# Kernel tuning notes

Measured on AMD Instinct MI355X. Metric: run time of the kernel, lower is better.

The kernel has to match this reference:

```python
import jax, jax.numpy as jnp
import numpy as np

N = 65536      # nodes
M = 65536      # memory nodes (== N, so no padding branch)
D = 256        # dim_model
H = 8          # heads
DK = D // H    # 32
DFF = 1024
E1 = 1048576   # intra edges
E2 = 524288    # inter edges
MAX_ETYPE = 1000
EPS = 1e-5
SCALE = 1.0 / float(np.sqrt(DK))


def layer_norm(x, g, b):
    mu = jnp.mean(x, axis=-1, keepdims=True)
    var = jnp.mean((x - mu) ** 2, axis=-1, keepdims=True)
    return (x - mu) * jax.lax.rsqrt(var + EPS) * g + b


def graph_attention(q, k, v, src, dst, n_dst, e_rel=None):
    # q: [Nq,H,DK]; k,v: [Nk,H,DK]; src/dst: [E]
    e = jnp.einsum('ehd,ehd->eh', k[src], q[dst])  # masked_mm
    if e_rel is not None:
        e = e + e_rel                               # node_mul_edge bias
    e = e * SCALE
    # segment softmax over incoming edges per destination (sparse_softmax)
    m = jax.ops.segment_max(e, dst, num_segments=n_dst)
    ex = jnp.exp(e - m[dst])
    denom = jax.ops.segment_sum(ex, dst, num_segments=n_dst)
    a = ex / denom[dst]                             # [E,H]
    # vec_spmm: aggregate a * v[src] into dst
    return jax.ops.segment_sum(a[:, :, None] * v[src], dst, num_segments=n_dst)


def setup_inputs() -> dict:
    key = jax.random.key(0)
    ks = jax.random.split(key, 24)
    w = lambda k, shp, fan: jax.random.normal(k, shp, jnp.float32) * (1.0 / np.sqrt(fan))
    inp = {
        'h': jax.random.normal(ks[0], (N, D), jnp.float32),
        'mem': jax.random.normal(ks[1], (M, D), jnp.float32),
        'src_intra': jax.random.randint(ks[2], (E1,), 0, N, jnp.int32),
        'dst_intra': jax.random.randint(ks[3], (E1,), 0, N, jnp.int32),
        'etype': jax.random.randint(ks[4], (E1,), 0, MAX_ETYPE, jnp.int32),
        'src_inter': jax.random.randint(ks[5], (E2,), 0, M, jnp.int32),
        'dst_inter': jax.random.randint(ks[6], (E2,), 0, N, jnp.int32),
        # intra-attention projections (branch 0)
        'Wq0': w(ks[7], (D, D), D), 'Wk0': w(ks[8], (D, D), D),
        'Wv0': w(ks[9], (D, D), D), 'Wo0': w(ks[10], (D, D), D),
        # inter-attention projections (branch 1)
        'Wq1': w(ks[11], (D, D), D), 'Wk1': w(ks[12], (D, D), D),
        'Wv1': w(ks[13], (D, D), D), 'Wo1': w(ks[14], (D, D), D),
        'ak_embed': jax.random.normal(ks[15], (MAX_ETYPE, DK), jnp.float32) * 0.02,
        # layer norms: norm_in[0], norm_in[1], norm_inter
        'ln0_g': jnp.ones((D,), jnp.float32), 'ln0_b': jnp.zeros((D,), jnp.float32),
        'ln1_g': jnp.ones((D,), jnp.float32), 'ln1_b': jnp.zeros((D,), jnp.float32),
        'ln2_g': jnp.ones((D,), jnp.float32), 'ln2_b': jnp.zeros((D,), jnp.float32),
        # FFN
        'Wf1': w(ks[16], (D, DFF), D), 'bf1': jnp.zeros((DFF,), jnp.float32),
        'Wf2': w(ks[17], (DFF, D), DFF), 'bf2': jnp.zeros((D,), jnp.float32),
    }
    return inp


def reference(h, mem, Wq0, Wk0, Wv0, Wo0, Wq1, Wk1, Wv1, Wo1, ak_embed,
              ln0_g, ln0_b, ln1_g, ln1_b, ln2_g, ln2_b,
              Wf1, bf1, Wf2, bf2,
              src_intra, dst_intra, etype, src_inter, dst_inter):
    # ---- intra (self) graph attention ----
    q = (h @ Wq0).reshape(-1, H, DK)
    k = (h @ Wk0).reshape(-1, H, DK)
    v = (h @ Wv0).reshape(-1, H, DK)
    ak = ak_embed[etype]                                   # [E1, DK]
    e_rel = jnp.einsum('ed,ehd->eh', ak, q[dst_intra])     # rel-pos bias
    a = graph_attention(q, k, v, src_intra, dst_intra, N, e_rel)
    o = a.reshape(-1, D) @ Wo0
    h = layer_norm(h + o, ln0_g, ln0_b)
    # ---- inter (memory) graph attention ----  (M == N: no padding)
    q = (h @ Wq1).reshape(-1, H, DK)
    k = (mem @ Wk1).reshape(-1, H, DK)
    v = (mem @ Wv1).reshape(-1, H, DK)
    a = graph_attention(q, k, v, src_inter, dst_inter, N)
    o = a.reshape(-1, D) @ Wo1
    h = layer_norm(h + o, ln1_g, ln1_b)
    # ---- FFN + norm_inter ----
    ffn = jax.nn.relu(h @ Wf1 + bf1) @ Wf2 + bf2
    h = layer_norm(h + ffn, ln2_g, ln2_b)
    return h
```

## Files before the change

### kernel.cpp

```cpp
#include <hip/hip_runtime.h>

#define N_NODES 65536
#define D_MODEL 256
#define DFF     1024
#define E1_N    1048576
#define E2_N    524288
#define ATT_SCALE 0.17677669529663687f
#define LN_EPS  1e-5f

#define NBUCK   128
#define BSHIFT  9
#define DPB     512

typedef __attribute__((ext_vector_type(8))) __bf16 bf16x8;
typedef __attribute__((ext_vector_type(4))) float  floatx4;
typedef __attribute__((ext_vector_type(4))) unsigned short ushortx4;
typedef __attribute__((ext_vector_type(8))) unsigned short ushortx8;

__device__ __forceinline__ float bf2f(unsigned short u) {
  return __uint_as_float(((unsigned)u) << 16);
}
__device__ __forceinline__ unsigned short f2bf(float f) {
  unsigned u = __float_as_uint(f);
  return (unsigned short)((u + 0x7FFFu + ((u >> 16) & 1u)) >> 16);
}
__device__ __forceinline__ int dot4i8(unsigned a, unsigned b, int c) {
#if __has_builtin(__builtin_amdgcn_sdot4)
  return __builtin_amdgcn_sdot4((int)a, (int)b, c, false);
#else
  c += (int)(signed char)(a & 0xFF) * (int)(signed char)(b & 0xFF);
  c += (int)(signed char)((a >> 8) & 0xFF) * (int)(signed char)((b >> 8) & 0xFF);
  c += (int)(signed char)((a >> 16) & 0xFF) * (int)(signed char)((b >> 16) & 0xFF);
  c += (int)(signed char)(a >> 24) * (int)(signed char)(b >> 24);
  return c;
#endif
}
__device__ __forceinline__ unsigned pack4i8(float a, float b, float c, float d, float inv) {
  int r0 = __float2int_rn(a * inv) & 0xFF;
  int r1 = __float2int_rn(b * inv) & 0xFF;
  int r2 = __float2int_rn(c * inv) & 0xFF;
  int r3 = __float2int_rn(d * inv) & 0xFF;
  return (unsigned)(r0 | (r1 << 8) | (r2 << 16) | (r3 << 24));
}

__device__ __forceinline__ void gld_lds16(const void* g, void* l) {
  __builtin_amdgcn_global_load_lds(
      (const __attribute__((address_space(1))) unsigned int*)g,
      (__attribute__((address_space(3))) unsigned int*)l, 16, 0, 0);
}

struct TW8 {
  const float* w[8];
  unsigned short* o[8];
};
__global__ __launch_bounds__(256) void transpose8(TW8 t) {
  __shared__ float tile[32][33];
  const int z = blockIdx.z;
  const float* W = t.w[z];
  unsigned short* Wt = t.o[z];
  const int tx = threadIdx.x & 31;
  const int ty = threadIdx.x >> 5;
  const int r0 = blockIdx.y * 32;
  const int c0 = blockIdx.x * 32;
#pragma unroll
  for (int p = 0; p < 4; ++p) {
    const int r = ty + p * 8;
    tile[r][tx] = W[(size_t)(r0 + r) * 256 + c0 + tx];
  }
  __syncthreads();
#pragma unroll
  for (int p = 0; p < 4; ++p) {
    const int r = ty + p * 8;
    Wt[(size_t)(c0 + r) * 256 + r0 + tx] = f2bf(tile[tx][r]);
  }
}

__global__ __launch_bounds__(256) void transpose_w(const float* __restrict__ W,
                                                   unsigned short* __restrict__ Wt,
                                                   int K, int Nc) {
  __shared__ float tile[32][33];
  const int tx = threadIdx.x & 31;
  const int ty = threadIdx.x >> 5;
  const int r0 = blockIdx.y * 32;
  const int c0 = blockIdx.x * 32;
#pragma unroll
  for (int p = 0; p < 4; ++p) {
    const int r = ty + p * 8;
    tile[r][tx] = W[(size_t)(r0 + r) * Nc + c0 + tx];
  }
  __syncthreads();
#pragma unroll
  for (int p = 0; p < 4; ++p) {
    const int r = ty + p * 8;
    Wt[(size_t)(c0 + r) * K + r0 + tx] = f2bf(tile[tx][r]);
  }
}

__global__ __launch_bounds__(256) void f2bf2_kernel(const float* __restrict__ in0,
                                                    unsigned short* __restrict__ out0,
                                                    const float* __restrict__ in1,
                                                    unsigned short* __restrict__ out1,
                                                    int half) {
  int i = blockIdx.x * 256 + threadIdx.x;
  const float* in = (i < half) ? in0 : in1;
  unsigned short* out = (i < half) ? out0 : out1;
  int k = (i < half) ? i : i - half;
  float4 v = ((const float4*)in)[k];
  ushortx4 o;
  o.x = f2bf(v.x); o.y = f2bf(v.y); o.z = f2bf(v.z); o.w = f2bf(v.w);
  ((ushortx4*)out)[k] = o;
}

__global__ __launch_bounds__(256) void zero_kernel(int* __restrict__ p, int n) {
  int i = blockIdx.x * 256 + threadIdx.x;
  if (i < n) p[i] = 0;
}


__global__ __launch_bounds__(256) void bucket_hist_kernel(const int* __restrict__ d0,
                                                          int* __restrict__ bh0,
                                                          const int* __restrict__ d1,
                                                          int* __restrict__ bh1) {
  __shared__ int h0[NBUCK], h1[NBUCK];
  const int tid = threadIdx.x;
  if (tid < NBUCK) { h0[tid] = 0; h1[tid] = 0; }
  __syncthreads();
  const int base = blockIdx.x * 2048;
#pragma unroll
  for (int i = 0; i < 8; ++i) {
    const int e = base + i * 256 + tid;
    atomicAdd(&h0[d0[e] >> BSHIFT], 1);
    if (e < E2_N) atomicAdd(&h1[d1[e] >> BSHIFT], 1);
  }
  __syncthreads();
  if (tid < NBUCK) {
    if (h0[tid]) atomicAdd(&bh0[tid], h0[tid]);
  } else if (tid < 2 * NBUCK) {
    const int t = tid - NBUCK;
    if (h1[t]) atomicAdd(&bh1[t], h1[t]);
  }
}

__global__ __launch_bounds__(256) void bucket_scan_kernel(const int* __restrict__ bh0,
                                                          int* __restrict__ bs0,
                                                          int* __restrict__ bc0,
                                                          int* __restrict__ rs0,
                                                          const int* __restrict__ bh1,
                                                          int* __restrict__ bs1,
                                                          int* __restrict__ bc1,
                                                          int* __restrict__ rs1) {
  __shared__ int l[2][NBUCK];
  const int tid = threadIdx.x;
  const int g = tid >> 7;
  const int t = tid & 127;
  const int* bh = g ? bh1 : bh0;
  int* bs = g ? bs1 : bs0;
  int* bc = g ? bc1 : bc0;
  const int orig = bh[t];
  int v = orig;
  l[g][t] = v;
  __syncthreads();
  for (int off = 1; off < NBUCK; off <<= 1) {
    const int add = (t >= off) ? l[g][t - off] : 0;
    __syncthreads();
    v += add;
    l[g][t] = v;
    __syncthreads();
  }
  bs[t + 1] = v;
  bc[t] = v - orig;
  if (t == 0) bs[0] = 0;
  if (tid == 0) rs0[N_NODES] = E1_N;
  if (tid == 1) rs1[N_NODES] = E2_N;
}

template <bool INTRA>
__global__ __launch_bounds__(256) void bin_kernel(const int* __restrict__ src,
                                                  const int* __restrict__ dst,
                                                  const int* __restrict__ et,
                                                  int* __restrict__ bcur,
                                                  void* __restrict__ outv) {
  __shared__ int cnt[NBUCK], gbase[NBUCK], lcur[NBUCK];
  const int tid = threadIdx.x;
  const int base = blockIdx.x * 2048;
  if (tid < NBUCK) { cnt[tid] = 0; lcur[tid] = 0; }
  int d[8], bk[8];
#pragma unroll
  for (int i = 0; i < 8; ++i) d[i] = dst[base + i * 256 + tid];
  __syncthreads();
#pragma unroll
  for (int i = 0; i < 8; ++i) {
    bk[i] = d[i] >> BSHIFT;
    atomicAdd(&cnt[bk[i]], 1);
  }
  __syncthreads();
  if (tid < NBUCK) gbase[tid] = atomicAdd(&bcur[tid], cnt[tid]);
  __syncthreads();
  if (INTRA) {
    int2* out = (int2*)outv;
#pragma unroll
    for (int i = 0; i < 8; ++i) {
      const int e = base + i * 256 + tid;
      const int loc = atomicAdd(&lcur[bk[i]], 1);
      out[gbase[bk[i]] + loc] = make_int2(src[e], (d[i] & (DPB - 1)) | (et[e] << 16));
    }
  } else {
    int* out = (int*)outv;
#pragma unroll
    for (int i = 0; i < 8; ++i) {
      const int e = base + i * 256 + tid;
      const int loc = atomicAdd(&lcur[bk[i]], 1);
      out[gbase[bk[i]] + loc] = src[e] | ((d[i] & (DPB - 1)) << 16);
    }
  }
}

__global__ __launch_bounds__(256) void csr_build_kernel(const int2* __restrict__ binned0,
                                                        const int* __restrict__ bs0,
                                                        int* __restrict__ rs0,
                                                        int2* __restrict__ out0,
                                                        const int* __restrict__ binned1,
                                                        const int* __restrict__ bs1,
                                                        int* __restrict__ rs1,
                                                        int* __restrict__ out1) {
  __shared__ int cnt[DPB];
  __shared__ int cur[DPB];
  __shared__ int wsum[4];
  const int tid = threadIdx.x;
  const int g = blockIdx.x >> 7;
  const int b = blockIdx.x & 127;
  const int bb = g ? bs1[b] : bs0[b];
  const int be = g ? bs1[b + 1] : bs0[b + 1];
  cnt[tid] = 0;
  cnt[tid + 256] = 0;
  __syncthreads();
  if (g == 0) {
    for (int j = bb + tid; j < be; j += 256) {
      atomicAdd(&cnt[binned0[j].y & (DPB - 1)], 1);
    }
  } else {
    for (int j = bb + tid; j < be; j += 256) {
      atomicAdd(&cnt[binned1[j] >> 16], 1);
    }
  }
  __syncthreads();
  const int lane = tid & 63;
  const int wv = tid >> 6;
  const int c0 = cnt[2 * tid];
  const int c1 = cnt[2 * tid + 1];
  const int s = c0 + c1;
  int incl = s;
#pragma unroll
  for (int m = 1; m < 64; m <<= 1) {
    const int u = __shfl_up(incl, m);
    if (lane >= m) incl += u;
  }
  if (lane == 63) wsum[wv] = incl;
  __syncthreads();
  int wb = 0;
  for (int w = 0; w < wv; ++w) wb += wsum[w];
  const int e0 = bb + wb + (incl - s);
  int* rs = g ? rs1 : rs0;
  rs[(b << BSHIFT) + 2 * tid] = e0;
  rs[(b << BSHIFT) + 2 * tid + 1] = e0 + c0;
  cur[2 * tid] = e0;
  cur[2 * tid + 1] = e0 + c0;
  __syncthreads();
  if (g == 0) {
    for (int j = bb + tid; j < be; j += 256) {
      const int2 w = binned0[j];
      const int p = atomicAdd(&cur[w.y & (DPB - 1)], 1);
      out0[p] = make_int2(w.x, w.y >> 16);
    }
  } else {
    for (int j = bb + tid; j < be; j += 256) {
      const int w = binned1[j];
      const int p = atomicAdd(&cur[w >> 16], 1);
      out1[p] = w & 0xFFFF;
    }
  }
}

template <bool BIAS, bool RELU, bool OUT_KVQ>
__global__ __launch_bounds__(256) void gemm_bf16(const unsigned short* __restrict__ A,
                                                 const unsigned short* __restrict__ Bt,
                                                 const float* __restrict__ bias,
                                                 void* __restrict__ C,
                                                 float* __restrict__ sbuf,
                                                 int K, int Ntot) {
  __shared__ __align__(16) unsigned short sA[128 * 32];
  __shared__ __align__(16) unsigned short sB[128 * 32];
  const int tid  = threadIdx.x;
  const int wave = tid >> 6;
  const int lane = tid & 63;
  const int m0 = blockIdx.y * 128;
  const int n0 = blockIdx.x * 128;

  floatx4 acc[4][4] = {};

  const int l4r = lane >> 2;
  const int l4c = (lane & 3) * 8;
  const int fr = lane & 15;
  const int fk = (lane >> 4) * 8;
  const int wy = (wave >> 1) * 64;
  const int wx = (wave & 1) * 64;

  for (int k0 = 0; k0 < K; k0 += 32) {
#pragma unroll
    for (int c = 0; c < 2; ++c) {
      const int row = wave * 32 + c * 16;
      gld_lds16(A  + ((size_t)(m0 + row + l4r) * K + k0 + l4c), &sA[row * 32]);
      gld_lds16(Bt + ((size_t)(n0 + row + l4r) * K + k0 + l4c), &sB[row * 32]);
    }
    __syncthreads();
    bf16x8 af[4], bfv[4];
#pragma unroll
    for (int i = 0; i < 4; ++i) af[i]  = *(const bf16x8*)&sA[(wy + i * 16 + fr) * 32 + fk];
#pragma unroll
    for (int j = 0; j < 4; ++j) bfv[j] = *(const bf16x8*)&sB[(wx + j * 16 + fr) * 32 + fk];
#pragma unroll
    for (int i = 0; i < 4; ++i)
#pragma unroll
      for (int j = 0; j < 4; ++j)
        acc[i][j] = __builtin_amdgcn_mfma_f32_16x16x32_bf16(af[i], bfv[j], acc[i][j], 0, 0, 0);
    __syncthreads();
  }

  const int coln = lane & 15;
  const int rowq = (lane >> 4) * 4;

  if (OUT_KVQ) {
    unsigned char* Cb = (unsigned char*)C;
#pragma unroll
    for (int i = 0; i < 4; ++i) {
#pragma unroll
      for (int jp = 0; jp < 2; ++jp) {
        const int head = ((n0 + wx) >> 5) + jp;
        const int pidx = (head < 8) ? head * 2 : (head - 8) * 2 + 1;
#pragma unroll
        for (int r = 0; r < 4; ++r) {
          float am = fmaxf(fabsf(acc[i][2 * jp][r]), fabsf(acc[i][2 * jp + 1][r]));
          am = fmaxf(am, __shfl_xor(am, 1));
          am = fmaxf(am, __shfl_xor(am, 2));
          am = fmaxf(am, __shfl_xor(am, 4));
          am = fmaxf(am, __shfl_xor(am, 8));
          const int m = m0 + wy + i * 16 + rowq + r;
          const float inv = am > 0.f ? 127.f / am : 0.f;
#pragma unroll
          for (int jj = 0; jj < 2; ++jj) {
            const int j = 2 * jp + jj;
            const int n = n0 + wx + j * 16 + coln;
            const int qv = __float2int_rn(acc[i][j][r] * inv);
            Cb[(size_t)m * 512 + n] = (unsigned char)(signed char)qv;
          }
          if (coln == 0) {
            sbuf[(size_t)m * 16 + pidx] = am * (1.f / 127.f);
          }
        }
      }
    }
  } else {
    unsigned short* Cs = (unsigned short*)C;
#pragma unroll
    for (int j = 0; j < 4; ++j) {
      const int n = n0 + wx + j * 16 + coln;
      float bval = 0.f;
      if (BIAS) bval = bias[n];
#pragma unroll
      for (int i = 0; i < 4; ++i) {
        const int mbase = m0 + wy + i * 16 + rowq;
#pragma unroll
        for (int r = 0; r < 4; ++r) {
          float v = acc[i][j][r] + bval;
          if (RELU) v = fmaxf(v, 0.f);
          Cs[(size_t)(mbase + r) * Ntot + n] = f2bf(v);
        }
      }
    }
  }
}

template <bool HAS_REL>
__global__ __launch_bounds__(256) void attn_kernel(const unsigned short* qb,
                                                   const unsigned char* __restrict__ kvb,
                                                   const float* __restrict__ sbuf,
                                                   const int* __restrict__ row_start,
                                                   const int2* __restrict__ s_se,
                                                   const int* __restrict__ s_src,
                                                   const float* __restrict__ ak_embed,
                                                   unsigned short* outp) {
  const int lane = threadIdx.x & 63;
  const int wave = threadIdx.x >> 6;
  const int dst  = blockIdx.x * 4 + wave;
  const int eg   = lane >> 4;
  const int l    = lane & 15;
  const int doff = l * 16;

  const unsigned short* qrow = qb + (size_t)dst * 256 + doff;
  ushortx8 qu0 = *(const ushortx8*)qrow;
  ushortx8 qu1 = *(const ushortx8*)(qrow + 8);
  float q[16];
#pragma unroll
  for (int d = 0; d < 8; ++d) {
    q[d]     = bf2f(qu0[d]) * ATT_SCALE;
    q[d + 8] = bf2f(qu1[d]) * ATT_SCALE;
  }
  float qam = 0.f;
#pragma unroll
  for (int d = 0; d < 16; ++d) qam = fmaxf(qam, fabsf(q[d]));
  qam = fmaxf(qam, __shfl_xor(qam, 1));
  const float qs   = qam * (1.f / 127.f);
  const float qinv = qam > 0.f ? 127.f / qam : 0.f;
  unsigned qi[4];
#pragma unroll
  for (int c = 0; c < 4; ++c)
    qi[c] = pack4i8(q[4 * c], q[4 * c + 1], q[4 * c + 2], q[4 * c + 3], qinv);

  float a[16];
#pragma unroll
  for (int d = 0; d < 16; ++d) a[d] = 0.f;
  float lsum = 0.f;

  const int beg = row_start[dst], end = row_start[dst + 1];
  for (int j = beg; j < end; j += 4) {
    const int e = j + eg;
    const bool valid = e < end;
    const int ecl = valid ? e : (end - 1);
    int src, et = 0;
    if (HAS_REL) {
      int2 se = s_se[ecl];
      src = se.x; et = se.y;
    } else {
      src = s_src[ecl];
    }
    const unsigned char* kvrow = kvb + (size_t)src * 512;
    float2 sc = *(const float2*)(sbuf + (size_t)src * 16 + (l >> 1) * 2);
    uint4 ku = *(const uint4*)(kvrow + doff);
    uint4 vu = *(const uint4*)(kvrow + 256 + doff);
    int idot = 0;
    idot = dot4i8(ku.x, qi[0], idot);
    idot = dot4i8(ku.y, qi[1], idot);
    idot = dot4i8(ku.z, qi[2], idot);
    idot = dot4i8(ku.w, qi[3], idot);
    float part = (float)idot * (sc.x * qs);
    if (HAS_REL) {
      const float* ak = ak_embed + (size_t)et * 32 + (l & 1) * 16;
      float4 a0 = *(const float4*)ak;
      float4 a1 = *(const float4*)(ak + 4);
      float4 a2 = *(const float4*)(ak + 8);
      float4 a3 = *(const float4*)(ak + 12);
      part += a0.x * q[0]  + a0.y * q[1]  + a0.z * q[2]  + a0.w * q[3]
            + a1.x * q[4]  + a1.y * q[5]  + a1.z * q[6]  + a1.w * q[7]
            + a2.x * q[8]  + a2.y * q[9]  + a2.z * q[10] + a2.w * q[11]
            + a3.x * q[12] + a3.y * q[13] + a3.z * q[14] + a3.w * q[15];
    }
    part += __shfl_xor(part, 1);
    const float pw = valid ? __expf(part) : 0.f;
    lsum += pw;
    const float pwv = pw * sc.y;
    {
      unsigned u = vu.x;
      a[0] += pwv * (float)(signed char)(u & 0xFF);
      a[1] += pwv * (float)(signed char)((u >> 8) & 0xFF);
      a[2] += pwv * (float)(signed char)((u >> 16) & 0xFF);
      a[3] += pwv * (float)(signed char)(u >> 24);
      u = vu.y;
      a[4] += pwv * (float)(signed char)(u & 0xFF);
      a[5] += pwv * (float)(signed char)((u >> 8) & 0xFF);
      a[6] += pwv * (float)(signed char)((u >> 16) & 0xFF);
      a[7] += pwv * (float)(signed char)(u >> 24);
      u = vu.z;
      a[8]  += pwv * (float)(signed char)(u & 0xFF);
      a[9]  += pwv * (float)(signed char)((u >> 8) & 0xFF);
      a[10] += pwv * (float)(signed char)((u >> 16) & 0xFF);
      a[11] += pwv * (float)(signed char)(u >> 24);
      u = vu.w;
      a[12] += pwv * (float)(signed char)(u & 0xFF);
      a[13] += pwv * (float)(signed char)((u >> 8) & 0xFF);
      a[14] += pwv * (float)(signed char)((u >> 16) & 0xFF);
      a[15] += pwv * (float)(signed char)(u >> 24);
    }
  }
  lsum += __shfl_xor(lsum, 16);
  lsum += __shfl_xor(lsum, 32);
#pragma unroll
  for (int d = 0; d < 16; ++d) {
    a[d] += __shfl_xor(a[d], 16);
    a[d] += __shfl_xor(a[d], 32);
  }
  const float inv = lsum > 0.f ? 1.f / lsum : 0.f;
  if (eg == 0) {
    ushortx8 o0, o1;
#pragma unroll
    for (int d = 0; d < 8; ++d) {
      o0[d] = f2bf(a[d] * inv);
      o1[d] = f2bf(a[d + 8] * inv);
    }
    unsigned short* orow = outp + (size_t)dst * 256 + doff;
    *(ushortx8*)orow = o0;
    *(ushortx8*)(orow + 8) = o1;
  }
}

template <bool WRITE_BF>
__global__ __launch_bounds__(256) void ln_kernel(const float* __restrict__ xin,
                                                 const unsigned short* __restrict__ oin,
                                                 const float* __restrict__ g,
                                                 const float* __restrict__ b,
                                                 float* __restrict__ xout,
                                                 unsigned short* __restrict__ bfout) {
  const int lane = threadIdx.x & 63;
  const int wave = threadIdx.x >> 6;
  const size_t row  = (size_t)blockIdx.x * 4 + wave;
  const size_t base = row * 256 + lane * 4;
  float4 xv = *(const float4*)(xin + base);
  ushortx4 ou = *(const ushortx4*)(oin + base);
  const float x0 = xv.x + bf2f(ou.x), x1 = xv.y + bf2f(ou.y),
              x2 = xv.z + bf2f(ou.z), x3 = xv.w + bf2f(ou.w);
  float sum = x0 + x1 + x2 + x3;
  float ss  = x0 * x0 + x1 * x1 + x2 * x2 + x3 * x3;
#pragma unroll
  for (int m = 1; m <= 32; m <<= 1) {
    sum += __shfl_xor(sum, m);
    ss  += __shfl_xor(ss, m);
  }
  const float mu  = sum * (1.f / 256.f);
  const float var = ss * (1.f / 256.f) - mu * mu;
  const float rs  = rsqrtf(var + LN_EPS);
  float4 gv = *(const float4*)(g + lane * 4);
  float4 bv = *(const float4*)(b + lane * 4);
  const float y0 = (x0 - mu) * rs * gv.x + bv.x;
  const float y1 = (x1 - mu) * rs * gv.y + bv.y;
  const float y2 = (x2 - mu) * rs * gv.z + bv.z;
  const float y3 = (x3 - mu) * rs * gv.w + bv.w;
  *(float4*)(xout + base) = make_float4(y0, y1, y2, y3);
  if (WRITE_BF) {
    ushortx4 yo;
    yo.x = f2bf(y0); yo.y = f2bf(y1); yo.z = f2bf(y2); yo.w = f2bf(y3);
    *(ushortx4*)(bfout + base) = yo;
  }
}

extern "C" void kernel_launch(void* const* d_in, const int* in_sizes, int n_in,
                              void* d_out, int out_size, void* d_ws, size_t ws_size,
                              hipStream_t stream) {
  const float* h_in      = (const float*)d_in[0];
  const float* mem_in    = (const float*)d_in[1];
  const int*   src_intra = (const int*)d_in[2];
  const int*   dst_intra = (const int*)d_in[3];
  const int*   etype     = (const int*)d_in[4];
  const int*   src_inter = (const int*)d_in[5];
  const int*   dst_inter = (const int*)d_in[6];
  const float* Wq0 = (const float*)d_in[7];
  const float* Wk0 = (const float*)d_in[8];
  const float* Wv0 = (const float*)d_in[9];
  const float* Wo0 = (const float*)d_in[10];
  const float* Wq1 = (const float*)d_in[11];
  const float* Wk1 = (const float*)d_in[12];
  const float* Wv1 = (const float*)d_in[13];
  const float* Wo1 = (const float*)d_in[14];
  const float* akE = (const float*)d_in[15];
  const float* ln0_g = (const float*)d_in[16];
  const float* ln0_b = (const float*)d_in[17];
  const float* ln1_g = (const float*)d_in[18];
  const float* ln1_b = (const float*)d_in[19];
  const float* ln2_g = (const float*)d_in[20];
  const float* ln2_b = (const float*)d_in[21];
  const float* Wf1 = (const float*)d_in[22];
  const float* bf1 = (const float*)d_in[23];
  const float* Wf2 = (const float*)d_in[24];
  const float* bf2 = (const float*)d_in[25];

  char* p = (char*)d_ws;
  auto alloc = [&](size_t bytes) {
    char* r = p;
    p += (bytes + 255) & ~(size_t)255;
    return r;
  };

  unsigned short* wqkv0t = (unsigned short*)alloc((size_t)768 * 256 * 2);
  unsigned short* wo0t   = (unsigned short*)alloc((size_t)256 * 256 * 2);
  unsigned short* wq1t   = (unsigned short*)alloc((size_t)256 * 256 * 2);
  unsigned short* wkv1t  = (unsigned short*)alloc((size_t)512 * 256 * 2);
  unsigned short* wo1t   = (unsigned short*)alloc((size_t)256 * 256 * 2);
  unsigned short* wf1t   = (unsigned short*)alloc((size_t)1024 * 256 * 2);
  unsigned short* wf2t   = (unsigned short*)alloc((size_t)256 * 1024 * 2);

  int* rs0   = (int*)alloc((size_t)(N_NODES + 1) * 4);
  int* rs1   = (int*)alloc((size_t)(N_NODES + 1) * 4);
  int2* sse0 = (int2*)alloc((size_t)E1_N * 8);
  int* ssrc1 = (int*)alloc((size_t)E2_N * 4);
  int* bh01 = (int*)alloc((size_t)2 * NBUCK * 4);
  int* bh0 = bh01;
  int* bh1 = bh01 + NBUCK;
  int* bs0 = (int*)alloc((size_t)(NBUCK + 1) * 4);
  int* bs1 = (int*)alloc((size_t)(NBUCK + 1) * 4);
  int* bc0 = (int*)alloc((size_t)NBUCK * 4);
  int* bc1 = (int*)alloc((size_t)NBUCK * 4);

  char* regionA = alloc((size_t)128 * 1024 * 1024);
  int2* binned0 = (int2*)regionA;
  int*  binned1 = (int*)(regionA + (size_t)E1_N * 8);
  unsigned short* qbuf    = (unsigned short*)regionA;
  unsigned char*  kv0q    = (unsigned char*)(regionA + (size_t)33554432);
  unsigned char*  kv1q    = (unsigned char*)(regionA + (size_t)67108864);
  unsigned short* scratch = (unsigned short*)(regionA + (size_t)100663296);
  unsigned short* hidden  = (unsigned short*)regionA;
  float* sbuf0 = (float*)alloc((size_t)N_NODES * 16 * 4);
  float* sbuf1 = (float*)alloc((size_t)N_NODES * 16 * 4);
  unsigned short* buf2 = (unsigned short*)alloc((size_t)N_NODES * 256 * 2);
  unsigned short* buf3 = (unsigned short*)alloc((size_t)N_NODES * 256 * 2);

  float* hcur = (float*)d_out;

  const int TB = 256;

  TW8 tw;
  tw.w[0] = Wq0; tw.o[0] = wqkv0t;
  tw.w[1] = Wk0; tw.o[1] = wqkv0t + 65536;
  tw.w[2] = Wv0; tw.o[2] = wqkv0t + 131072;
  tw.w[3] = Wo0; tw.o[3] = wo0t;
  tw.w[4] = Wq1; tw.o[4] = wq1t;
  tw.w[5] = Wk1; tw.o[5] = wkv1t;
  tw.w[6] = Wv1; tw.o[6] = wkv1t + 65536;
  tw.w[7] = Wo1; tw.o[7] = wo1t;
  transpose8<<<dim3(8, 8, 8), TB, 0, stream>>>(tw);
  transpose_w<<<dim3(32, 8), TB, 0, stream>>>(Wf1, wf1t, 256, 1024);
  transpose_w<<<dim3(8, 32), TB, 0, stream>>>(Wf2, wf2t, 1024, 256);

  f2bf2_kernel<<<32768, TB, 0, stream>>>(h_in, buf2, mem_in, buf3, N_NODES * 256 / 4);

  zero_kernel<<<1, TB, 0, stream>>>(bh01, 2 * NBUCK);
  bucket_hist_kernel<<<E1_N / 2048, TB, 0, stream>>>(dst_intra, bh0, dst_inter, bh1);
  bucket_scan_kernel<<<1, TB, 0, stream>>>(bh0, bs0, bc0, rs0, bh1, bs1, bc1, rs1);
  bin_kernel<true><<<E1_N / 2048, TB, 0, stream>>>(src_intra, dst_intra, etype, bc0, binned0);
  bin_kernel<false><<<E2_N / 2048, TB, 0, stream>>>(src_inter, dst_inter, nullptr, bc1, binned1);
  csr_build_kernel<<<2 * NBUCK, TB, 0, stream>>>(binned0, bs0, rs0, sse0,
                                                 binned1, bs1, rs1, ssrc1);

  gemm_bf16<false, false, false><<<dim3(2, 512), TB, 0, stream>>>(buf2, wqkv0t, nullptr, qbuf, nullptr, 256, 256);
  gemm_bf16<false, false, true><<<dim3(4, 512), TB, 0, stream>>>(buf2, wqkv0t + 65536, nullptr, kv0q, sbuf0, 256, 512);
  attn_kernel<true><<<16384, TB, 0, stream>>>(qbuf, kv0q, sbuf0, rs0, sse0, nullptr, akE, qbuf);
  gemm_bf16<false, false, false><<<dim3(2, 512), TB, 0, stream>>>(qbuf, wo0t, nullptr, scratch, nullptr, 256, 256);
  ln_kernel<true><<<16384, TB, 0, stream>>>(h_in, scratch, ln0_g, ln0_b, hcur, buf2);

  gemm_bf16<false, false, false><<<dim3(2, 512), TB, 0, stream>>>(buf2, wq1t, nullptr, qbuf, nullptr, 256, 256);
  gemm_bf16<false, false, true><<<dim3(4, 512), TB, 0, stream>>>(buf3, wkv1t, nullptr, kv1q, sbuf1, 256, 512);
  attn_kernel<false><<<16384, TB, 0, stream>>>(qbuf, kv1q, sbuf1, rs1, nullptr, ssrc1, nullptr, qbuf);
  gemm_bf16<false, false, false><<<dim3(2, 512), TB, 0, stream>>>(qbuf, wo1t, nullptr, scratch, nullptr, 256, 256);
  ln_kernel<true><<<16384, TB, 0, stream>>>(hcur, scratch, ln1_g, ln1_b, hcur, buf3);

  gemm_bf16<true, true, false><<<dim3(8, 512), TB, 0, stream>>>(buf3, wf1t, bf1, hidden, nullptr, 256, 1024);
  gemm_bf16<true, false, false><<<dim3(2, 512), TB, 0, stream>>>(hidden, wf2t, bf2, buf2, nullptr, 1024, 256);
  ln_kernel<false><<<16384, TB, 0, stream>>>(hcur, buf2, ln2_g, ln2_b, hcur, nullptr);
}
```

Before: 881.1 us.

## Fuse Q/KV projection GEMMs, quantize rel-pos embed, software-pipeline attention gathers

Merges the Q and KV projection GEMMs into one launch that picks the operand by block column. V is now stored as biased uint8 so the attention loop can unpack it with plain shifts, and the bias is removed at the end via a running weight sum. The relative-position embedding is quantized to int8 once so its bias term becomes a dot4 on the already-quantized q. The attention edge loop now prefetches the next edge's indices and K/V payload, and destinations with no incoming edges exit early. The int8 embedding adds some quantization error, and the prefetch raises register pressure.

```diff
diff --git a/kernel.cpp b/kernel.cpp
--- a/kernel.cpp
+++ b/kernel.cpp
@@ -5,6 +5,7 @@
 #define DFF     1024
 #define E1_N    1048576
 #define E2_N    524288
+#define METYPE  1000
 #define ATT_SCALE 0.17677669529663687f
 #define LN_EPS  1e-5f
 
@@ -116,6 +117,34 @@
   if (i < n) p[i] = 0;
 }
 
+__global__ __launch_bounds__(256) void quant_ak_kernel(const float* __restrict__ ak,
+                                                       unsigned char* __restrict__ ak8,
+                                                       float* __restrict__ aks) {
+  const int r = blockIdx.x * 256 + threadIdx.x;
+  if (r >= METYPE) return;
+  const float* row = ak + (size_t)r * 32;
+  float v[32];
+  float am = 0.f;
+#pragma unroll
+  for (int i = 0; i < 32; ++i) {
+    v[i] = row[i];
+    am = fmaxf(am, fabsf(v[i]));
+  }
+  const float inv = am > 0.f ? 127.f / am : 0.f;
+  uint4 o0, o1;
+  o0.x = pack4i8(v[0], v[1], v[2], v[3], inv);
+  o0.y = pack4i8(v[4], v[5], v[6], v[7], inv);
+  o0.z = pack4i8(v[8], v[9], v[10], v[11], inv);
+  o0.w = pack4i8(v[12], v[13], v[14], v[15], inv);
+  o1.x = pack4i8(v[16], v[17], v[18], v[19], inv);
+  o1.y = pack4i8(v[20], v[21], v[22], v[23], inv);
+  o1.z = pack4i8(v[24], v[25], v[26], v[27], inv);
+  o1.w = pack4i8(v[28], v[29], v[30], v[31], inv);
+  uint4* out = (uint4*)(ak8 + (size_t)r * 32);
+  out[0] = o0;
+  out[1] = o1;
+  aks[r] = am * (1.f / 127.f);
+}
 
 __global__ __launch_bounds__(256) void bucket_hist_kernel(const int* __restrict__ d0,
                                                           int* __restrict__ bh0,
@@ -281,12 +310,11 @@
   }
 }
 
-template <bool BIAS, bool RELU, bool OUT_KVQ>
+template <bool BIAS, bool RELU>
 __global__ __launch_bounds__(256) void gemm_bf16(const unsigned short* __restrict__ A,
                                                  const unsigned short* __restrict__ Bt,
                                                  const float* __restrict__ bias,
-                                                 void* __restrict__ C,
-                                                 float* __restrict__ sbuf,
+                                                 unsigned short* __restrict__ C,
                                                  int K, int Ntot) {
   __shared__ __align__(16) unsigned short sA[128 * 32];
   __shared__ __align__(16) unsigned short sB[128 * 32];
@@ -328,15 +356,96 @@
 
   const int coln = lane & 15;
   const int rowq = (lane >> 4) * 4;
-
-  if (OUT_KVQ) {
-    unsigned char* Cb = (unsigned char*)C;
+#pragma unroll
+  for (int j = 0; j < 4; ++j) {
+    const int n = n0 + wx + j * 16 + coln;
+    float bval = 0.f;
+    if (BIAS) bval = bias[n];
+#pragma unroll
+    for (int i = 0; i < 4; ++i) {
+      const int mbase = m0 + wy + i * 16 + rowq;
+#pragma unroll
+      for (int r = 0; r < 4; ++r) {
+        float v = acc[i][j][r] + bval;
+        if (RELU) v = fmaxf(v, 0.f);
+        C[(size_t)(mbase + r) * Ntot + n] = f2bf(v);
+      }
+    }
+  }
+}
+
+__global__ __launch_bounds__(256) void gemm_qkv(const unsigned short* __restrict__ Aq,
+                                                const unsigned short* __restrict__ Btq,
+                                                unsigned short* __restrict__ Cq,
+                                                const unsigned short* __restrict__ Akv,
+                                                const unsigned short* __restrict__ Btkv,
+                                                unsigned char* __restrict__ Ckv,
+                                                float* __restrict__ sbuf) {
+  __shared__ __align__(16) unsigned short sA[128 * 32];
+  __shared__ __align__(16) unsigned short sB[128 * 32];
+  const int tid  = threadIdx.x;
+  const int wave = tid >> 6;
+  const int lane = tid & 63;
+  const bool isq = blockIdx.x < 2;
+  const unsigned short* A  = isq ? Aq : Akv;
+  const unsigned short* Bt = isq ? Btq : Btkv;
+  const int m0 = blockIdx.y * 128;
+  const int n0 = (isq ? blockIdx.x : (blockIdx.x - 2)) * 128;
+
+  floatx4 acc[4][4] = {};
+
+  const int l4r = lane >> 2;
+  const int l4c = (lane & 3) * 8;
+  const int fr = lane & 15;
+  const int fk = (lane >> 4) * 8;
+  const int wy = (wave >> 1) * 64;
+  const int wx = (wave & 1) * 64;
+
+  for (int k0 = 0; k0 < 256; k0 += 32) {
+#pragma unroll
+    for (int c = 0; c < 2; ++c) {
+      const int row = wave * 32 + c * 16;
+      gld_lds16(A  + ((size_t)(m0 + row + l4r) * 256 + k0 + l4c), &sA[row * 32]);
+      gld_lds16(Bt + ((size_t)(n0 + row + l4r) * 256 + k0 + l4c), &sB[row * 32]);
+    }
+    __syncthreads();
+    bf16x8 af[4], bfv[4];
+#pragma unroll
+    for (int i = 0; i < 4; ++i) af[i]  = *(const bf16x8*)&sA[(wy + i * 16 + fr) * 32 + fk];
+#pragma unroll
+    for (int j = 0; j < 4; ++j) bfv[j] = *(const bf16x8*)&sB[(wx + j * 16 + fr) * 32 + fk];
+#pragma unroll
+    for (int i = 0; i < 4; ++i)
+#pragma unroll
+      for (int j = 0; j < 4; ++j)
+        acc[i][j] = __builtin_amdgcn_mfma_f32_16x16x32_bf16(af[i], bfv[j], acc[i][j], 0, 0, 0);
+    __syncthreads();
+  }
+
+  const int coln = lane & 15;
+  const int rowq = (lane >> 4) * 4;
+
+  if (isq) {
+#pragma unroll
+    for (int j = 0; j < 4; ++j) {
+      const int n = n0 + wx + j * 16 + coln;
+#pragma unroll
+      for (int i = 0; i < 4; ++i) {
+        const int mbase = m0 + wy + i * 16 + rowq;
+#pragma unroll
+        for (int r = 0; r < 4; ++r) {
+          Cq[(size_t)(mbase + r) * 256 + n] = f2bf(acc[i][j][r]);
+        }
+      }
+    }
+  } else {
 #pragma unroll
     for (int i = 0; i < 4; ++i) {
 #pragma unroll
       for (int jp = 0; jp < 2; ++jp) {
         const int head = ((n0 + wx) >> 5) + jp;
         const int pidx = (head < 8) ? head * 2 : (head - 8) * 2 + 1;
+        const bool isv = head >= 8;
 #pragma unroll
         for (int r = 0; r < 4; ++r) {
           float am = fmaxf(fabsf(acc[i][2 * jp][r]), fabsf(acc[i][2 * jp + 1][r]));
@@ -351,29 +460,12 @@
             const int j = 2 * jp + jj;
             const int n = n0 + wx + j * 16 + coln;
             const int qv = __float2int_rn(acc[i][j][r] * inv);
-            Cb[(size_t)m * 512 + n] = (unsigned char)(signed char)qv;
+            Ckv[(size_t)m * 512 + n] =
+                isv ? (unsigned char)(qv + 128) : (unsigned char)(signed char)qv;
           }
           if (coln == 0) {
             sbuf[(size_t)m * 16 + pidx] = am * (1.f / 127.f);
           }
-        }
-      }
-    }
-  } else {
-    unsigned short* Cs = (unsigned short*)C;
-#pragma unroll
-    for (int j = 0; j < 4; ++j) {
-      const int n = n0 + wx + j * 16 + coln;
-      float bval = 0.f;
-      if (BIAS) bval = bias[n];
-#pragma unroll
-      for (int i = 0; i < 4; ++i) {
-        const int mbase = m0 + wy + i * 16 + rowq;
-#pragma unroll
-        for (int r = 0; r < 4; ++r) {
-          float v = acc[i][j][r] + bval;
-          if (RELU) v = fmaxf(v, 0.f);
-          Cs[(size_t)(mbase + r) * Ntot + n] = f2bf(v);
         }
       }
     }
@@ -387,7 +479,8 @@
                                                    const int* __restrict__ row_start,
                                                    const int2* __restrict__ s_se,
                                                    const int* __restrict__ s_src,
-                                                   const float* __restrict__ ak_embed,
+                                                   const unsigned char* __restrict__ ak8,
+                                                   const float* __restrict__ aks,
                                                    unsigned short* outp) {
   const int lane = threadIdx.x & 63;
   const int wave = threadIdx.x >> 6;
@@ -396,6 +489,17 @@
   const int l    = lane & 15;
   const int doff = l * 16;
 
+  const int beg = row_start[dst], end = row_start[dst + 1];
+  unsigned short* orow = outp + (size_t)dst * 256 + doff;
+  if (beg >= end) {
+    if (eg == 0) {
+      ushortx8 z = {};
+      *(ushortx8*)orow = z;
+      *(ushortx8*)(orow + 8) = z;
+    }
+    return;
+  }
+
   const unsigned short* qrow = qb + (size_t)dst * 256 + doff;
   ushortx8 qu0 = *(const ushortx8*)qrow;
   ushortx8 qu1 = *(const ushortx8*)(qrow + 8);
@@ -419,68 +523,91 @@
   float a[16];
 #pragma unroll
   for (int d = 0; d < 16; ++d) a[d] = 0.f;
-  float lsum = 0.f;
-
-  const int beg = row_start[dst], end = row_start[dst + 1];
-  for (int j = beg; j < end; j += 4) {
-    const int e = j + eg;
-    const bool valid = e < end;
-    const int ecl = valid ? e : (end - 1);
-    int src, et = 0;
+  float lsum = 0.f, pwvsum = 0.f;
+
+  auto ldse = [&](int j) -> int2 {
+    const int ecl = min(j + eg, end - 1);
+    if (HAS_REL) return s_se[ecl];
+    return make_int2(s_src[ecl], 0);
+  };
+  auto ldpay = [&](int2 se, float2& sc, uint4& ku, uint4& vu, uint4& ak, float& ax) {
+    const unsigned char* kvrow = kvb + (size_t)se.x * 512;
+    sc = *(const float2*)(sbuf + (size_t)se.x * 16 + (l >> 1) * 2);
+    ku = *(const uint4*)(kvrow + doff);
+    vu = *(const uint4*)(kvrow + 256 + doff);
     if (HAS_REL) {
-      int2 se = s_se[ecl];
-      src = se.x; et = se.y;
-    } else {
-      src = s_src[ecl];
-    }
-    const unsigned char* kvrow = kvb + (size_t)src * 512;
-    float2 sc = *(const float2*)(sbuf + (size_t)src * 16 + (l >> 1) * 2);
-    uint4 ku = *(const uint4*)(kvrow + doff);
-    uint4 vu = *(const uint4*)(kvrow + 256 + doff);
-    int idot = 0;
-    idot = dot4i8(ku.x, qi[0], idot);
-    idot = dot4i8(ku.y, qi[1], idot);
-    idot = dot4i8(ku.z, qi[2], idot);
-    idot = dot4i8(ku.w, qi[3], idot);
-    float part = (float)idot * (sc.x * qs);
-    if (HAS_REL) {
-      const float* ak = ak_embed + (size_t)et * 32 + (l & 1) * 16;
-      float4 a0 = *(const float4*)ak;
-      float4 a1 = *(const float4*)(ak + 4);
-      float4 a2 = *(const float4*)(ak + 8);
-      float4 a3 = *(const float4*)(ak + 12);
-      part += a0.x * q[0]  + a0.y * q[1]  + a0.z * q[2]  + a0.w * q[3]
-            + a1.x * q[4]  + a1.y * q[5]  + a1.z * q[6]  + a1.w * q[7]
-            + a2.x * q[8]  + a2.y * q[9]  + a2.z * q[10] + a2.w * q[11]
-            + a3.x * q[12] + a3.y * q[13] + a3.z * q[14] + a3.w * q[15];
-    }
-    part += __shfl_xor(part, 1);
-    const float pw = valid ? __expf(part) : 0.f;
-    lsum += pw;
-    const float pwv = pw * sc.y;
+      ak = *(const uint4*)(ak8 + (size_t)se.y * 32 + (l & 1) * 16);
+      ax = aks[se.y];
+    }
+  };
+
+  int2 se_c = ldse(beg);
+  float2 sc_c;
+  uint4 ku_c, vu_c, ak_c;
+  float aks_c;
+  ldpay(se_c, sc_c, ku_c, vu_c, ak_c, aks_c);
+  int2 se_n = ldse(beg + 4);
+
+  int j = beg;
+  while (true) {
+    const bool more = (j + 4) < end;
+    float2 sc_n;
+    uint4 ku_n, vu_n, ak_n;
+    float aks_n;
+    int2 se_nn;
+    if (more) {
+      ldpay(se_n, sc_n, ku_n, vu_n, ak_n, aks_n);
+      se_nn = ldse(j + 8);
+    }
     {
-      unsigned u = vu.x;
-      a[0] += pwv * (float)(signed char)(u & 0xFF);
-      a[1] += pwv * (float)(signed char)((u >> 8) & 0xFF);
-      a[2] += pwv * (float)(signed char)((u >> 16) & 0xFF);
-      a[3] += pwv * (float)(signed char)(u >> 24);
-      u = vu.y;
-      a[4] += pwv * (float)(signed char)(u & 0xFF);
-      a[5] += pwv * (float)(signed char)((u >> 8) & 0xFF);
-      a[6] += pwv * (float)(signed char)((u >> 16) & 0xFF);
-      a[7] += pwv * (float)(signed char)(u >> 24);
-      u = vu.z;
-      a[8]  += pwv * (float)(signed char)(u & 0xFF);
-      a[9]  += pwv * (float)(signed char)((u >> 8) & 0xFF);
-      a[10] += pwv * (float)(signed char)((u >> 16) & 0xFF);
-      a[11] += pwv * (float)(signed char)(u >> 24);
-      u = vu.w;
-      a[12] += pwv * (float)(signed char)(u & 0xFF);
-      a[13] += pwv * (float)(signed char)((u >> 8) & 0xFF);
-      a[14] += pwv * (float)(signed char)((u >> 16) & 0xFF);
-      a[15] += pwv * (float)(signed char)(u >> 24);
-    }
-  }
+      const bool valid = (j + eg) < end;
+      int id = 0;
+      id = dot4i8(ku_c.x, qi[0], id);
+      id = dot4i8(ku_c.y, qi[1], id);
+      id = dot4i8(ku_c.z, qi[2], id);
+      id = dot4i8(ku_c.w, qi[3], id);
+      float sco = (float)id * sc_c.x;
+      if (HAS_REL) {
+        int ib = 0;
+        ib = dot4i8(ak_c.x, qi[0], ib);
+        ib = dot4i8(ak_c.y, qi[1], ib);
+        ib = dot4i8(ak_c.z, qi[2], ib);
+        ib = dot4i8(ak_c.w, qi[3], ib);
+        sco = fmaf((float)ib, aks_c, sco);
+      }
+      float part = sco * qs;
+      part += __shfl_xor(part, 1);
+      const float pw = valid ? __expf(part) : 0.f;
+      lsum += pw;
+      const float pwv = pw * sc_c.y;
+      pwvsum += pwv;
+      a[0]  += pwv * (float)(vu_c.x & 0xFFu);
+      a[1]  += pwv * (float)((vu_c.x >> 8) & 0xFFu);
+      a[2]  += pwv * (float)((vu_c.x >> 16) & 0xFFu);
+      a[3]  += pwv * (float)(vu_c.x >> 24);
+      a[4]  += pwv * (float)(vu_c.y & 0xFFu);
+      a[5]  += pwv * (float)((vu_c.y >> 8) & 0xFFu);
+      a[6]  += pwv * (float)((vu_c.y >> 16) & 0xFFu);
+      a[7]  += pwv * (float)(vu_c.y >> 24);
+      a[8]  += pwv * (float)(vu_c.z & 0xFFu);
+      a[9]  += pwv * (float)((vu_c.z >> 8) & 0xFFu);
+      a[10] += pwv * (float)((vu_c.z >> 16) & 0xFFu);
+      a[11] += pwv * (float)(vu_c.z >> 24);
+      a[12] += pwv * (float)(vu_c.w & 0xFFu);
+      a[13] += pwv * (float)((vu_c.w >> 8) & 0xFFu);
+      a[14] += pwv * (float)((vu_c.w >> 16) & 0xFFu);
+      a[15] += pwv * (float)(vu_c.w >> 24);
+    }
+    if (!more) break;
+    se_c = se_n; se_n = se_nn;
+    sc_c = sc_n; ku_c = ku_n; vu_c = vu_n;
+    ak_c = ak_n; aks_c = aks_n;
+    j += 4;
+  }
+
+#pragma unroll
+  for (int d = 0; d < 16; ++d) a[d] = fmaf(-128.f, pwvsum, a[d]);
+
   lsum += __shfl_xor(lsum, 16);
   lsum += __shfl_xor(lsum, 32);
 #pragma unroll
@@ -496,7 +623,6 @@
       o0[d] = f2bf(a[d] * inv);
       o1[d] = f2bf(a[d + 8] * inv);
     }
-    unsigned short* orow = outp + (size_t)dst * 256 + doff;
     *(ushortx8*)orow = o0;
     *(ushortx8*)(orow + 8) = o1;
   }
@@ -597,6 +723,8 @@
   int* bs1 = (int*)alloc((size_t)(NBUCK + 1) * 4);
   int* bc0 = (int*)alloc((size_t)NBUCK * 4);
   int* bc1 = (int*)alloc((size_t)NBUCK * 4);
+  unsigned char* ak8 = (unsigned char*)alloc((size_t)METYPE * 32);
+  float* aksb = (float*)alloc((size_t)METYPE * 4);
 
   char* regionA = alloc((size_t)128 * 1024 * 1024);
   int2* binned0 = (int2*)regionA;
@@ -627,6 +755,7 @@
   transpose8<<<dim3(8, 8, 8), TB, 0, stream>>>(tw);
   transpose_w<<<dim3(32, 8), TB, 0, stream>>>(Wf1, wf1t, 256, 1024);
   transpose_w<<<dim3(8, 32), TB, 0, stream>>>(Wf2, wf2t, 1024, 256);
+  quant_ak_kernel<<<4, TB, 0, stream>>>(akE, ak8, aksb);
 
   f2bf2_kernel<<<32768, TB, 0, stream>>>(h_in, buf2, mem_in, buf3, N_NODES * 256 / 4);
 
@@ -638,19 +767,21 @@
   csr_build_kernel<<<2 * NBUCK, TB, 0, stream>>>(binned0, bs0, rs0, sse0,
                                                  binned1, bs1, rs1, ssrc1);
 
-  gemm_bf16<false, false, false><<<dim3(2, 512), TB, 0, stream>>>(buf2, wqkv0t, nullptr, qbuf, nullptr, 256, 256);
-  gemm_bf16<false, false, true><<<dim3(4, 512), TB, 0, stream>>>(buf2, wqkv0t + 65536, nullptr, kv0q, sbuf0, 256, 512);
-  attn_kernel<true><<<16384, TB, 0, stream>>>(qbuf, kv0q, sbuf0, rs0, sse0, nullptr, akE, qbuf);
-  gemm_bf16<false, false, false><<<dim3(2, 512), TB, 0, stream>>>(qbuf, wo0t, nullptr, scratch, nullptr, 256, 256);
+  gemm_qkv<<<dim3(6, 512), TB, 0, stream>>>(buf2, wqkv0t, qbuf,
+                                            buf2, wqkv0t + 65536, kv0q, sbuf0);
+  attn_kernel<true><<<16384, TB, 0, stream>>>(qbuf, kv0q, sbuf0, rs0, sse0, nullptr,
+                                              ak8, aksb, qbuf);
+  gemm_bf16<false, false><<<dim3(2, 512), TB, 0, stream>>>(qbuf, wo0t, nullptr, scratch, 256, 256);
   ln_kernel<true><<<16384, TB, 0, stream>>>(h_in, scratch, ln0_g, ln0_b, hcur, buf2);
 
-  gemm_bf16<false, false, false><<<dim3(2, 512), TB, 0, stream>>>(buf2, wq1t, nullptr, qbuf, nullptr, 256, 256);
-  gemm_bf16<false, false, true><<<dim3(4, 512), TB, 0, stream>>>(buf3, wkv1t, nullptr, kv1q, sbuf1, 256, 512);
-  attn_kernel<false><<<16384, TB, 0, stream>>>(qbuf, kv1q, sbuf1, rs1, nullptr, ssrc1, nullptr, qbuf);
-  gemm_bf16<false, false, false><<<dim3(2, 512), TB, 0, stream>>>(qbuf, wo1t, nullptr, scratch, nullptr, 256, 256);
+  gemm_qkv<<<dim3(6, 512), TB, 0, stream>>>(buf2, wq1t, qbuf,
+                                            buf3, wkv1t, kv1q, sbuf1);
+  attn_kernel<false><<<16384, TB, 0, stream>>>(qbuf, kv1q, sbuf1, rs1, nullptr, ssrc1,
+                                               nullptr, nullptr, qbuf);
+  gemm_bf16<false, false><<<dim3(2, 512), TB, 0, stream>>>(qbuf, wo1t, nullptr, scratch, 256, 256);
   ln_kernel<true><<<16384, TB, 0, stream>>>(hcur, scratch, ln1_g, ln1_b, hcur, buf3);
 
-  gemm_bf16<true, true, false><<<dim3(8, 512), TB, 0, stream>>>(buf3, wf1t, bf1, hidden, nullptr, 256, 1024);
-  gemm_bf16<true, false, false><<<dim3(2, 512), TB, 0, stream>>>(hidden, wf2t, bf2, buf2, nullptr, 1024, 256);
+  gemm_bf16<true, true><<<dim3(8, 512), TB, 0, stream>>>(buf3, wf1t, bf1, hidden, 256, 1024);
+  gemm_bf16<true, false><<<dim3(2, 512), TB, 0, stream>>>(hidden, wf2t, bf2, buf2, 1024, 256);
   ln_kernel<false><<<16384, TB, 0, stream>>>(hcur, buf2, ln2_g, ln2_b, hcur, nullptr);
 }
```

New measurement: 845.8 us. 1.04x faster.
